# Performance work log

Measured on AMD Instinct MI355X. Metric: run time of the kernel, lower is better.

Reference implementation:

```python
import jax, jax.numpy as jnp
import numpy as np

V, D, H, HA = 10000, 1024, 1024, 128  # ntoken, ninp, nhid, adapt hidden
T, B = 128, 64


def setup_inputs() -> dict:
    key = jax.random.key(0)
    ks = jax.random.split(key, 8)
    u = lambda k, sh, r: jax.random.uniform(k, sh, jnp.float32, -r, r)
    return {
        "tokens": jax.random.randint(ks[0], (T, B), 0, V, dtype=jnp.int32),
        "emb": u(ks[1], (V, D), 0.1),                 # encoder weight, uniform(-0.1,0.1)
        "Wax": u(ks[2], (D, HA), 1.0 / np.sqrt(D)),   # adapt_module input weight
        "Wah": u(ks[3], (HA, HA), 1.0 / np.sqrt(HA)), # adapt_module recurrent weight
        "bah": jnp.zeros((HA,), jnp.float32),
        "Wa": u(ks[4], (HA, 2), 1.0 / np.sqrt(HA)),   # readout -> (n, s)
        "ba": jnp.zeros((2,), jnp.float32),
        "Wih": u(ks[5], (D, H), 1.0 / np.sqrt(D)),    # gamma_rnn input weight
        "Whh": u(ks[6], (H, H), 1.0 / np.sqrt(H)),    # gamma_rnn recurrent weight
        "bh": jnp.zeros((H,), jnp.float32),
        "Wd": u(ks[7], (H, V), 0.1),                  # decoder weight, uniform(-0.1,0.1)
        "bd": jnp.zeros((V,), jnp.float32),           # decoder bias, zeros
    }


def reference(tokens, emb, Wax, Wah, bah, Wa, ba, Wih, Whh, bh, Wd, bd):
    x = emb[tokens]  # [T, B, D] embedding lookup (encoder)
    Bsz = tokens.shape[1]

    def step(carry, x_t):
        h0, h1 = carry
        # adapt_module: small RNN producing per-sample gates a = [n, s]
        h0n = jnp.tanh(x_t @ Wax + h0 @ Wah + bah)            # [B, HA]
        a = jax.nn.sigmoid(h0n @ Wa + ba)                      # [B, 2]
        n, s = a[:, 0:1], a[:, 1:2]
        # gamma_rnn: adaptive-activation vanilla RNN cell
        pre = x_t @ Wih + h1 @ Whh + bh                        # [B, H]
        h1n = (1.0 - s) * jnp.tanh(n * pre) + s * jax.nn.sigmoid(n * pre)
        return (h0n, h1n), h1n

    h0_0 = jnp.zeros((Bsz, HA), x.dtype)
    h1_0 = jnp.zeros((Bsz, H), x.dtype)
    (_, h1_final), hs = jax.lax.scan(step, (h0_0, h1_0), x)   # hs: [T, B, H]
    decoded = hs @ Wd + bd                                     # [T, B, V]
    return decoded, h1_final
```

## Files before the change

### kernel.cpp

```cpp
#include <hip/hip_runtime.h>
#include <hip/hip_bf16.h>
#include <cstdint>
#include <cstddef>

#define TSTEPS 128
#define BATCH  64
#define DDIM   1024
#define HDIM   1024
#define HADIM  128
#define VOCAB  10000
#define MROWS  (TSTEPS * BATCH)

typedef __attribute__((ext_vector_type(8))) short bf16x8;
typedef __attribute__((ext_vector_type(4))) float f32x4;

__device__ __forceinline__ unsigned short f2bf(float x) {
    unsigned int u = __float_as_uint(x);
    unsigned int r = (u + 0x7fffu + ((u >> 16) & 1u)) >> 16;
    return (unsigned short)r;
}

__global__ __launch_bounds__(256) void transpose_cast(const float* __restrict__ W,
                                                      unsigned short* __restrict__ Wt,
                                                      int R, int C) {
    __shared__ float tile[32][33];
    int tc = blockIdx.x * 32;
    int tr = blockIdx.y * 32;
    int tid = threadIdx.x;
    for (int i = 0; i < 4; i++) {
        int idx = tid + i * 256;
        int r = idx >> 5, c = idx & 31;
        float v = 0.f;
        if (tr + r < R && tc + c < C) v = W[(size_t)(tr + r) * C + tc + c];
        tile[r][c] = v;
    }
    __syncthreads();
    for (int i = 0; i < 4; i++) {
        int idx = tid + i * 256;
        int r = idx >> 5, c = idx & 31;
        if (tc + r < C && tr + c < R)
            Wt[(size_t)(tc + r) * R + tr + c] = f2bf(tile[c][r]);
    }
}

__global__ __launch_bounds__(256) void gather_cast(const int* __restrict__ tok,
                                                   const float* __restrict__ emb,
                                                   unsigned short* __restrict__ xb) {
    int i = blockIdx.x;
    int t = tok[i];
    const float4* src = (const float4*)(emb + (size_t)t * DDIM);
    float4 v = src[threadIdx.x];
    ushort4 o;
    o.x = f2bf(v.x); o.y = f2bf(v.y); o.z = f2bf(v.z); o.w = f2bf(v.w);
    ((ushort4*)(xb + (size_t)i * DDIM))[threadIdx.x] = o;
}

__global__ __launch_bounds__(256) void zero_ushort(unsigned short* p, int n) {
    int i = blockIdx.x * 256 + threadIdx.x;
    if (i < n) p[i] = 0;
}

__global__ __launch_bounds__(256) void gemm_bt_bias(const unsigned short* __restrict__ A,
                                                    const unsigned short* __restrict__ Bt,
                                                    const float* __restrict__ bias,
                                                    float* __restrict__ C,
                                                    int M, int N, int K) {
    __shared__ unsigned short As[64 * 40];
    __shared__ unsigned short Bs[64 * 40];
    int rowBase = blockIdx.y * 64;
    int colBase = blockIdx.x * 64;
    int tid = threadIdx.x;
    int wave = tid >> 6, lane = tid & 63;
    int wr = wave >> 1, wc = wave & 1;
    int quad = lane >> 4, lr = lane & 15;
    int ldRow = tid >> 2;
    int ldK = (tid & 3) * 8;
    bool bvalid = (colBase + ldRow) < N;
    const unsigned short* Ag = A + (size_t)(rowBase + ldRow) * K + ldK;
    const unsigned short* Bg = Bt + (size_t)(colBase + ldRow) * K + ldK;

    f32x4 acc[2][2] = {};
    for (int k0 = 0; k0 < K; k0 += 32) {
        uint4 av = *(const uint4*)(Ag + k0);
        uint4 bv = {};
        if (bvalid) bv = *(const uint4*)(Bg + k0);
        __syncthreads();
        *(uint4*)(As + ldRow * 40 + ldK) = av;
        *(uint4*)(Bs + ldRow * 40 + ldK) = bv;
        __syncthreads();
        bf16x8 a0 = *(const bf16x8*)(As + (wr * 32 + lr) * 40 + quad * 8);
        bf16x8 a1 = *(const bf16x8*)(As + (wr * 32 + 16 + lr) * 40 + quad * 8);
        bf16x8 b0 = *(const bf16x8*)(Bs + (wc * 32 + lr) * 40 + quad * 8);
        bf16x8 b1 = *(const bf16x8*)(Bs + (wc * 32 + 16 + lr) * 40 + quad * 8);
        acc[0][0] = __builtin_amdgcn_mfma_f32_16x16x32_bf16(a0, b0, acc[0][0], 0, 0, 0);
        acc[0][1] = __builtin_amdgcn_mfma_f32_16x16x32_bf16(a0, b1, acc[0][1], 0, 0, 0);
        acc[1][0] = __builtin_amdgcn_mfma_f32_16x16x32_bf16(a1, b0, acc[1][0], 0, 0, 0);
        acc[1][1] = __builtin_amdgcn_mfma_f32_16x16x32_bf16(a1, b1, acc[1][1], 0, 0, 0);
    }
    for (int mi = 0; mi < 2; mi++)
        for (int ni = 0; ni < 2; ni++) {
            int col = colBase + wc * 32 + ni * 16 + lr;
            if (col < N) {
                float b = bias[col];
                for (int r = 0; r < 4; r++) {
                    int row = rowBase + wr * 32 + mi * 16 + quad * 4 + r;
                    C[(size_t)row * N + col] = acc[mi][ni][r] + b;
                }
            }
        }
}

__global__ __launch_bounds__(128) void h0_chain(const float* __restrict__ Xa,
                                                const float* __restrict__ Wah,
                                                const float* __restrict__ Wa,
                                                const float* __restrict__ ba,
                                                float2* __restrict__ ns) {
    int b = blockIdx.x;
    int j = threadIdx.x;
    __shared__ float WahS[HADIM * HADIM];
    __shared__ float h0s[HADIM];
    __shared__ float red[4];
    for (int i = j; i < HADIM * HADIM; i += 128) WahS[i] = Wah[i];
    h0s[j] = 0.f;
    float wa0 = Wa[j * 2 + 0], wa1 = Wa[j * 2 + 1];
    float ba0 = ba[0], ba1 = ba[1];
    __syncthreads();
    for (int t = 0; t < TSTEPS; t++) {
        float acc = Xa[((size_t)t * BATCH + b) * HADIM + j];
        for (int k = 0; k < HADIM; k++) acc += h0s[k] * WahS[k * HADIM + j];
        float h0n = tanhf(acc);
        float p0 = h0n * wa0, p1 = h0n * wa1;
        for (int off = 32; off > 0; off >>= 1) {
            p0 += __shfl_down(p0, off);
            p1 += __shfl_down(p1, off);
        }
        int wv = j >> 6;
        if ((j & 63) == 0) { red[wv * 2 + 0] = p0; red[wv * 2 + 1] = p1; }
        __syncthreads();
        float n = 1.f / (1.f + __expf(-(red[0] + red[2] + ba0)));
        float s = 1.f / (1.f + __expf(-(red[1] + red[3] + ba1)));
        if (j == 0) ns[t * BATCH + b] = make_float2(n, s);
        h0s[j] = h0n;
        __syncthreads();
    }
}

__global__ __launch_bounds__(64) void rnn_step(const unsigned short* __restrict__ Aprev,
                                               const unsigned short* __restrict__ WhhT,
                                               const float* __restrict__ Xi_t,
                                               const float2* __restrict__ ns_t,
                                               unsigned short* __restrict__ hs_t,
                                               float* __restrict__ h1f) {
    __shared__ unsigned short As[16 * 72];
    __shared__ unsigned short Bs[16 * 72];
    int rg = blockIdx.x & 3;
    int cg = blockIdx.x >> 2;
    int lane = threadIdx.x;
    int quad = lane >> 4, lr = lane & 15;
    int ldRow = lane >> 2;
    int ldK = (lane & 3) * 16;
    const unsigned short* Ag = Aprev + (size_t)(rg * 16 + ldRow) * HDIM + ldK;
    const unsigned short* Bg = WhhT + (size_t)(cg * 16 + ldRow) * HDIM + ldK;

    f32x4 acc = {};
    uint4 a0 = *(const uint4*)(Ag);
    uint4 a1 = *(const uint4*)(Ag + 8);
    uint4 b0 = *(const uint4*)(Bg);
    uint4 b1 = *(const uint4*)(Bg + 8);
    for (int k0 = 0; k0 < HDIM; k0 += 64) {
        __syncthreads();
        *(uint4*)(As + ldRow * 72 + ldK) = a0;
        *(uint4*)(As + ldRow * 72 + ldK + 8) = a1;
        *(uint4*)(Bs + ldRow * 72 + ldK) = b0;
        *(uint4*)(Bs + ldRow * 72 + ldK + 8) = b1;
        __syncthreads();
        if (k0 + 64 < HDIM) {
            a0 = *(const uint4*)(Ag + k0 + 64);
            a1 = *(const uint4*)(Ag + k0 + 72);
            b0 = *(const uint4*)(Bg + k0 + 64);
            b1 = *(const uint4*)(Bg + k0 + 72);
        }
        bf16x8 af0 = *(const bf16x8*)(As + lr * 72 + quad * 8);
        bf16x8 bf0 = *(const bf16x8*)(Bs + lr * 72 + quad * 8);
        bf16x8 af1 = *(const bf16x8*)(As + lr * 72 + 32 + quad * 8);
        bf16x8 bf1 = *(const bf16x8*)(Bs + lr * 72 + 32 + quad * 8);
        acc = __builtin_amdgcn_mfma_f32_16x16x32_bf16(af0, bf0, acc, 0, 0, 0);
        acc = __builtin_amdgcn_mfma_f32_16x16x32_bf16(af1, bf1, acc, 0, 0, 0);
    }
    int col = cg * 16 + lr;
    for (int r = 0; r < 4; r++) {
        int brow = rg * 16 + quad * 4 + r;
        float2 g = ns_t[brow];
        float pre = acc[r] + Xi_t[(size_t)brow * HDIM + col];
        float z = g.x * pre;
        float th = tanhf(z);
        float sg = 1.f / (1.f + __expf(-z));
        float h1n = (1.f - g.y) * th + g.y * sg;
        hs_t[(size_t)brow * HDIM + col] = f2bf(h1n);
        h1f[(size_t)brow * HDIM + col] = h1n;
    }
}

extern "C" void kernel_launch(void* const* d_in, const int* in_sizes, int n_in,
                              void* d_out, int out_size, void* d_ws, size_t ws_size,
                              hipStream_t stream) {
    const int*   tokens = (const int*)d_in[0];
    const float* emb    = (const float*)d_in[1];
    const float* Wax    = (const float*)d_in[2];
    const float* Wah    = (const float*)d_in[3];
    const float* bah    = (const float*)d_in[4];
    const float* Wa     = (const float*)d_in[5];
    const float* ba     = (const float*)d_in[6];
    const float* Wih    = (const float*)d_in[7];
    const float* Whh    = (const float*)d_in[8];
    const float* bh     = (const float*)d_in[9];
    const float* Wd     = (const float*)d_in[10];
    const float* bd     = (const float*)d_in[11];
    float* out = (float*)d_out;

    char* ws = (char*)d_ws;
    size_t off = 0;
    auto alloc = [&](size_t bytes) -> void* {
        void* p = ws + off;
        off += (bytes + 255) & ~(size_t)255;
        return p;
    };
    unsigned short* WihT = (unsigned short*)alloc((size_t)HDIM * DDIM * 2);
    unsigned short* WaxT = (unsigned short*)alloc((size_t)HADIM * DDIM * 2);
    unsigned short* WhhT = (unsigned short*)alloc((size_t)HDIM * HDIM * 2);
    unsigned short* WdT  = (unsigned short*)alloc((size_t)VOCAB * HDIM * 2);
    unsigned short* xb   = (unsigned short*)alloc((size_t)MROWS * DDIM * 2);
    float*          Xi   = (float*)alloc((size_t)MROWS * HDIM * 4);
    float*          Xa   = (float*)alloc((size_t)MROWS * HADIM * 4);
    unsigned short* hs   = (unsigned short*)alloc((size_t)MROWS * HDIM * 2);
    float2*         ns   = (float2*)alloc((size_t)TSTEPS * BATCH * 8);
    unsigned short* zerosA = (unsigned short*)alloc((size_t)BATCH * HDIM * 2);
    float*          h1scr  = (float*)alloc((size_t)BATCH * HDIM * 4);

    transpose_cast<<<dim3(32, 32), 256, 0, stream>>>(Wih, WihT, DDIM, HDIM);
    transpose_cast<<<dim3(4, 32), 256, 0, stream>>>(Wax, WaxT, DDIM, HADIM);
    transpose_cast<<<dim3(32, 32), 256, 0, stream>>>(Whh, WhhT, HDIM, HDIM);
    transpose_cast<<<dim3(313, 32), 256, 0, stream>>>(Wd, WdT, HDIM, VOCAB);
    gather_cast<<<MROWS, 256, 0, stream>>>(tokens, emb, xb);
    zero_ushort<<<(BATCH * HDIM + 255) / 256, 256, 0, stream>>>(zerosA, BATCH * HDIM);
    gemm_bt_bias<<<dim3(HDIM / 64, MROWS / 64), 256, 0, stream>>>(xb, WihT, bh, Xi, MROWS, HDIM, DDIM);
    gemm_bt_bias<<<dim3(HADIM / 64, MROWS / 64), 256, 0, stream>>>(xb, WaxT, bah, Xa, MROWS, HADIM, DDIM);
    h0_chain<<<BATCH, 128, 0, stream>>>(Xa, Wah, Wa, ba, ns);
    for (int t = 0; t < TSTEPS; t++) {
        const unsigned short* Ap = (t == 0) ? zerosA : hs + (size_t)(t - 1) * BATCH * HDIM;
        float* h1f = (t == TSTEPS - 1) ? (out + (size_t)MROWS * VOCAB) : h1scr;
        rnn_step<<<256, 64, 0, stream>>>(Ap, WhhT, Xi + (size_t)t * BATCH * HDIM,
                                         ns + t * BATCH, hs + (size_t)t * BATCH * HDIM, h1f);
    }
    gemm_bt_bias<<<dim3((VOCAB + 63) / 64, MROWS / 64), 256, 0, stream>>>(hs, WdT, bd, out, MROWS, VOCAB, HDIM);
}
```

Measured before the change: 2.347 ms.

## Replace per-step RNN launches with persistent kernel and enlarge GEMM tiles

Replaces the 128 per-timestep rnn_step launches with one persistent kernel of 64 blocks. Each block keeps its 16-column slice of Whh in LDS and the blocks synchronise between timesteps through a global atomic barrier, which removes launch overhead and the repeated weight loads. The GEMMs move to 128x128 tiles with register prefetch of the next K slice, giving more reuse per block. The grid barrier assumes all 64 blocks are resident at once, and the recurrence now runs on only 64 blocks.

```diff
diff --git a/kernel.cpp b/kernel.cpp
--- a/kernel.cpp
+++ b/kernel.cpp
@@ -55,56 +55,73 @@
     ((ushort4*)(xb + (size_t)i * DDIM))[threadIdx.x] = o;
 }
 
-__global__ __launch_bounds__(256) void zero_ushort(unsigned short* p, int n) {
+__global__ __launch_bounds__(256) void zero_u32(unsigned int* p, int n) {
     int i = blockIdx.x * 256 + threadIdx.x;
-    if (i < n) p[i] = 0;
-}
-
-__global__ __launch_bounds__(256) void gemm_bt_bias(const unsigned short* __restrict__ A,
-                                                    const unsigned short* __restrict__ Bt,
-                                                    const float* __restrict__ bias,
-                                                    float* __restrict__ C,
-                                                    int M, int N, int K) {
-    __shared__ unsigned short As[64 * 40];
-    __shared__ unsigned short Bs[64 * 40];
-    int rowBase = blockIdx.y * 64;
-    int colBase = blockIdx.x * 64;
-    int tid = threadIdx.x;
-    int wave = tid >> 6, lane = tid & 63;
-    int wr = wave >> 1, wc = wave & 1;
-    int quad = lane >> 4, lr = lane & 15;
-    int ldRow = tid >> 2;
-    int ldK = (tid & 3) * 8;
-    bool bvalid = (colBase + ldRow) < N;
-    const unsigned short* Ag = A + (size_t)(rowBase + ldRow) * K + ldK;
-    const unsigned short* Bg = Bt + (size_t)(colBase + ldRow) * K + ldK;
-
-    f32x4 acc[2][2] = {};
+    if (i < n) p[i] = 0u;
+}
+
+__global__ __launch_bounds__(256) void gemm128(const unsigned short* __restrict__ A,
+                                               const unsigned short* __restrict__ Bt,
+                                               const float* __restrict__ bias,
+                                               float* __restrict__ C,
+                                               int M, int N, int K) {
+    __shared__ unsigned short As[128 * 40];
+    __shared__ unsigned short Bs[128 * 40];
+    const int tid = threadIdx.x;
+    const int wave = tid >> 6, lane = tid & 63;
+    const int wr = wave >> 1, wc = wave & 1;
+    const int quad = lane >> 4, lr = lane & 15;
+    const int rowBase = blockIdx.x * 128;
+    const int colBase = blockIdx.y * 128;
+    const int sr = tid >> 2;
+    const int sk = (tid & 3) * 8;
+    const unsigned short* Ag0 = A + (size_t)(rowBase + sr) * K + sk;
+    const unsigned short* Ag1 = Ag0 + (size_t)64 * K;
+    int cb0 = colBase + sr;      if (cb0 > N - 1) cb0 = N - 1;
+    int cb1 = colBase + 64 + sr; if (cb1 > N - 1) cb1 = N - 1;
+    const unsigned short* Bg0 = Bt + (size_t)cb0 * K + sk;
+    const unsigned short* Bg1 = Bt + (size_t)cb1 * K + sk;
+
+    f32x4 acc[4][4] = {};
+    uint4 a0 = *(const uint4*)Ag0, a1 = *(const uint4*)Ag1;
+    uint4 b0 = *(const uint4*)Bg0, b1 = *(const uint4*)Bg1;
     for (int k0 = 0; k0 < K; k0 += 32) {
-        uint4 av = *(const uint4*)(Ag + k0);
-        uint4 bv = {};
-        if (bvalid) bv = *(const uint4*)(Bg + k0);
-        __syncthreads();
-        *(uint4*)(As + ldRow * 40 + ldK) = av;
-        *(uint4*)(Bs + ldRow * 40 + ldK) = bv;
-        __syncthreads();
-        bf16x8 a0 = *(const bf16x8*)(As + (wr * 32 + lr) * 40 + quad * 8);
-        bf16x8 a1 = *(const bf16x8*)(As + (wr * 32 + 16 + lr) * 40 + quad * 8);
-        bf16x8 b0 = *(const bf16x8*)(Bs + (wc * 32 + lr) * 40 + quad * 8);
-        bf16x8 b1 = *(const bf16x8*)(Bs + (wc * 32 + 16 + lr) * 40 + quad * 8);
-        acc[0][0] = __builtin_amdgcn_mfma_f32_16x16x32_bf16(a0, b0, acc[0][0], 0, 0, 0);
-        acc[0][1] = __builtin_amdgcn_mfma_f32_16x16x32_bf16(a0, b1, acc[0][1], 0, 0, 0);
-        acc[1][0] = __builtin_amdgcn_mfma_f32_16x16x32_bf16(a1, b0, acc[1][0], 0, 0, 0);
-        acc[1][1] = __builtin_amdgcn_mfma_f32_16x16x32_bf16(a1, b1, acc[1][1], 0, 0, 0);
-    }
-    for (int mi = 0; mi < 2; mi++)
-        for (int ni = 0; ni < 2; ni++) {
-            int col = colBase + wc * 32 + ni * 16 + lr;
+        __syncthreads();
+        *(uint4*)&As[sr * 40 + sk] = a0;
+        *(uint4*)&As[(64 + sr) * 40 + sk] = a1;
+        *(uint4*)&Bs[sr * 40 + sk] = b0;
+        *(uint4*)&Bs[(64 + sr) * 40 + sk] = b1;
+        __syncthreads();
+        int kn = k0 + 32;
+        if (kn < K) {
+            a0 = *(const uint4*)(Ag0 + kn);
+            a1 = *(const uint4*)(Ag1 + kn);
+            b0 = *(const uint4*)(Bg0 + kn);
+            b1 = *(const uint4*)(Bg1 + kn);
+        }
+        bf16x8 af[4], bfr[4];
+        #pragma unroll
+        for (int i = 0; i < 4; i++) {
+            af[i]  = *(const bf16x8*)&As[(wr * 64 + i * 16 + lr) * 40 + quad * 8];
+            bfr[i] = *(const bf16x8*)&Bs[(wc * 64 + i * 16 + lr) * 40 + quad * 8];
+        }
+        #pragma unroll
+        for (int mi = 0; mi < 4; mi++)
+            #pragma unroll
+            for (int ni = 0; ni < 4; ni++)
+                acc[mi][ni] = __builtin_amdgcn_mfma_f32_16x16x32_bf16(af[mi], bfr[ni], acc[mi][ni], 0, 0, 0);
+    }
+    #pragma unroll
+    for (int mi = 0; mi < 4; mi++)
+        #pragma unroll
+        for (int ni = 0; ni < 4; ni++) {
+            int col = colBase + wc * 64 + ni * 16 + lr;
             if (col < N) {
-                float b = bias[col];
+                float bv = bias[col];
+                #pragma unroll
                 for (int r = 0; r < 4; r++) {
-                    int row = rowBase + wr * 32 + mi * 16 + quad * 4 + r;
-                    C[(size_t)row * N + col] = acc[mi][ni][r] + b;
+                    int row = rowBase + wr * 64 + mi * 16 + quad * 4 + r;
+                    C[(size_t)row * N + col] = acc[mi][ni][r] + bv;
                 }
             }
         }
@@ -145,59 +162,68 @@
     }
 }
 
-__global__ __launch_bounds__(64) void rnn_step(const unsigned short* __restrict__ Aprev,
-                                               const unsigned short* __restrict__ WhhT,
-                                               const float* __restrict__ Xi_t,
-                                               const float2* __restrict__ ns_t,
-                                               unsigned short* __restrict__ hs_t,
-                                               float* __restrict__ h1f) {
-    __shared__ unsigned short As[16 * 72];
-    __shared__ unsigned short Bs[16 * 72];
-    int rg = blockIdx.x & 3;
-    int cg = blockIdx.x >> 2;
-    int lane = threadIdx.x;
-    int quad = lane >> 4, lr = lane & 15;
-    int ldRow = lane >> 2;
-    int ldK = (lane & 3) * 16;
-    const unsigned short* Ag = Aprev + (size_t)(rg * 16 + ldRow) * HDIM + ldK;
-    const unsigned short* Bg = WhhT + (size_t)(cg * 16 + ldRow) * HDIM + ldK;
-
-    f32x4 acc = {};
-    uint4 a0 = *(const uint4*)(Ag);
-    uint4 a1 = *(const uint4*)(Ag + 8);
-    uint4 b0 = *(const uint4*)(Bg);
-    uint4 b1 = *(const uint4*)(Bg + 8);
-    for (int k0 = 0; k0 < HDIM; k0 += 64) {
-        __syncthreads();
-        *(uint4*)(As + ldRow * 72 + ldK) = a0;
-        *(uint4*)(As + ldRow * 72 + ldK + 8) = a1;
-        *(uint4*)(Bs + ldRow * 72 + ldK) = b0;
-        *(uint4*)(Bs + ldRow * 72 + ldK + 8) = b1;
-        __syncthreads();
-        if (k0 + 64 < HDIM) {
-            a0 = *(const uint4*)(Ag + k0 + 64);
-            a1 = *(const uint4*)(Ag + k0 + 72);
-            b0 = *(const uint4*)(Bg + k0 + 64);
-            b1 = *(const uint4*)(Bg + k0 + 72);
-        }
-        bf16x8 af0 = *(const bf16x8*)(As + lr * 72 + quad * 8);
-        bf16x8 bf0 = *(const bf16x8*)(Bs + lr * 72 + quad * 8);
-        bf16x8 af1 = *(const bf16x8*)(As + lr * 72 + 32 + quad * 8);
-        bf16x8 bf1 = *(const bf16x8*)(Bs + lr * 72 + 32 + quad * 8);
-        acc = __builtin_amdgcn_mfma_f32_16x16x32_bf16(af0, bf0, acc, 0, 0, 0);
-        acc = __builtin_amdgcn_mfma_f32_16x16x32_bf16(af1, bf1, acc, 0, 0, 0);
-    }
-    int col = cg * 16 + lr;
-    for (int r = 0; r < 4; r++) {
-        int brow = rg * 16 + quad * 4 + r;
-        float2 g = ns_t[brow];
-        float pre = acc[r] + Xi_t[(size_t)brow * HDIM + col];
-        float z = g.x * pre;
-        float th = tanhf(z);
-        float sg = 1.f / (1.f + __expf(-z));
-        float h1n = (1.f - g.y) * th + g.y * sg;
-        hs_t[(size_t)brow * HDIM + col] = f2bf(h1n);
-        h1f[(size_t)brow * HDIM + col] = h1n;
+__global__ __launch_bounds__(256) void rnn_persist(const unsigned short* __restrict__ WhhT,
+                                                   const float* __restrict__ Xi,
+                                                   const float2* __restrict__ ns,
+                                                   unsigned short* __restrict__ hs,
+                                                   float* __restrict__ h1f,
+                                                   unsigned int* __restrict__ bar) {
+    __shared__ unsigned short Bsl[16 * 1032];
+    const int w = blockIdx.x;
+    const int tid = threadIdx.x;
+    const int wave = tid >> 6, lane = tid & 63;
+    const int quad = lane >> 4, lr = lane & 15;
+    for (int i = tid; i < 16 * 128; i += 256) {
+        int r = i >> 7, k = (i & 127) * 8;
+        *(uint4*)&Bsl[r * 1032 + k] = *(const uint4*)&WhhT[(size_t)(w * 16 + r) * HDIM + k];
+    }
+    __syncthreads();
+    const int col = w * 16 + lr;
+    const int mrow = wave * 16 + lr;
+    for (int t = 0; t < TSTEPS; t++) {
+        const float* Xit = Xi + (size_t)t * BATCH * HDIM;
+        float xi[4]; float2 g[4];
+        #pragma unroll
+        for (int r = 0; r < 4; r++) {
+            int brow = wave * 16 + quad * 4 + r;
+            xi[r] = Xit[(size_t)brow * HDIM + col];
+            g[r] = ns[t * BATCH + brow];
+        }
+        f32x4 acc = {};
+        if (t > 0) {
+            const unsigned short* Ap = hs + (size_t)(t - 1) * BATCH * HDIM
+                                          + (size_t)mrow * HDIM + quad * 8;
+            const unsigned short* Bp = (const unsigned short*)Bsl + lr * 1032 + quad * 8;
+            #pragma unroll 8
+            for (int k0 = 0; k0 < HDIM; k0 += 32) {
+                bf16x8 av = *(const bf16x8*)(Ap + k0);
+                bf16x8 bv = *(const bf16x8*)(Bp + k0);
+                acc = __builtin_amdgcn_mfma_f32_16x16x32_bf16(av, bv, acc, 0, 0, 0);
+            }
+        }
+        unsigned short* hst = hs + (size_t)t * BATCH * HDIM;
+        #pragma unroll
+        for (int r = 0; r < 4; r++) {
+            int brow = wave * 16 + quad * 4 + r;
+            float pre = acc[r] + xi[r];
+            float z = g[r].x * pre;
+            float th = tanhf(z);
+            float sg = 1.f / (1.f + __expf(-z));
+            float h1n = (1.f - g[r].y) * th + g[r].y * sg;
+            hst[(size_t)brow * HDIM + col] = f2bf(h1n);
+            if (t == TSTEPS - 1) h1f[(size_t)brow * HDIM + col] = h1n;
+        }
+        if (t < TSTEPS - 1) {
+            __threadfence();
+            __syncthreads();
+            if (tid == 0) {
+                __hip_atomic_fetch_add(&bar[t], 1u, __ATOMIC_RELEASE, __HIP_MEMORY_SCOPE_AGENT);
+                while (__hip_atomic_load(&bar[t], __ATOMIC_RELAXED, __HIP_MEMORY_SCOPE_AGENT) < 64u)
+                    __builtin_amdgcn_s_sleep(1);
+            }
+            __syncthreads();
+            __threadfence();
+        }
     }
 }
 
@@ -234,23 +260,17 @@
     float*          Xa   = (float*)alloc((size_t)MROWS * HADIM * 4);
     unsigned short* hs   = (unsigned short*)alloc((size_t)MROWS * HDIM * 2);
     float2*         ns   = (float2*)alloc((size_t)TSTEPS * BATCH * 8);
-    unsigned short* zerosA = (unsigned short*)alloc((size_t)BATCH * HDIM * 2);
-    float*          h1scr  = (float*)alloc((size_t)BATCH * HDIM * 4);
+    unsigned int*   bar  = (unsigned int*)alloc((size_t)TSTEPS * 4);
 
     transpose_cast<<<dim3(32, 32), 256, 0, stream>>>(Wih, WihT, DDIM, HDIM);
     transpose_cast<<<dim3(4, 32), 256, 0, stream>>>(Wax, WaxT, DDIM, HADIM);
     transpose_cast<<<dim3(32, 32), 256, 0, stream>>>(Whh, WhhT, HDIM, HDIM);
     transpose_cast<<<dim3(313, 32), 256, 0, stream>>>(Wd, WdT, HDIM, VOCAB);
     gather_cast<<<MROWS, 256, 0, stream>>>(tokens, emb, xb);
-    zero_ushort<<<(BATCH * HDIM + 255) / 256, 256, 0, stream>>>(zerosA, BATCH * HDIM);
-    gemm_bt_bias<<<dim3(HDIM / 64, MROWS / 64), 256, 0, stream>>>(xb, WihT, bh, Xi, MROWS, HDIM, DDIM);
-    gemm_bt_bias<<<dim3(HADIM / 64, MROWS / 64), 256, 0, stream>>>(xb, WaxT, bah, Xa, MROWS, HADIM, DDIM);
+    zero_u32<<<1, 256, 0, stream>>>(bar, TSTEPS);
+    gemm128<<<dim3(MROWS / 128, 1), 256, 0, stream>>>(xb, WaxT, bah, Xa, MROWS, HADIM, DDIM);
     h0_chain<<<BATCH, 128, 0, stream>>>(Xa, Wah, Wa, ba, ns);
-    for (int t = 0; t < TSTEPS; t++) {
-        const unsigned short* Ap = (t == 0) ? zerosA : hs + (size_t)(t - 1) * BATCH * HDIM;
-        float* h1f = (t == TSTEPS - 1) ? (out + (size_t)MROWS * VOCAB) : h1scr;
-        rnn_step<<<256, 64, 0, stream>>>(Ap, WhhT, Xi + (size_t)t * BATCH * HDIM,
-                                         ns + t * BATCH, hs + (size_t)t * BATCH * HDIM, h1f);
-    }
-    gemm_bt_bias<<<dim3((VOCAB + 63) / 64, MROWS / 64), 256, 0, stream>>>(hs, WdT, bd, out, MROWS, VOCAB, HDIM);
-}
+    gemm128<<<dim3(MROWS / 128, HDIM / 128), 256, 0, stream>>>(xb, WihT, bh, Xi, MROWS, HDIM, DDIM);
+    rnn_persist<<<64, 256, 0, stream>>>(WhhT, Xi, ns, hs, out + (size_t)MROWS * VOCAB, bar);
+    gemm128<<<dim3(MROWS / 128, (VOCAB + 127) / 128), 256, 0, stream>>>(hs, WdT, bd, out, MROWS, VOCAB, HDIM);
+}
```

Measured after the change: 3.033 ms. 29.2% more time.
